# Kernel optimization log

Hardware: AMD Instinct MI355X
Metric: run time of the kernel (lower is better)

The kernel has to match this reference:

```python
import jax, jax.numpy as jnp
import numpy as np

B, N_NUC, N_UP, N_DOWN = 512, 16, 32, 32
N_ELEC = N_UP + N_DOWN            # 64 electrons
F = 8                             # edge feature dim (Gaussian RBF envelopes)
D = N_NUC * F                     # embedding_dim = 128 (positional electron embeddings)
L = 3                             # n_interactions
N_ATOM_TYPES = 4


def _rbf(diff):
    # diff: [..., 3] -> [..., F]; Gaussian RBF features of the interparticle distance
    d = jnp.sqrt(jnp.sum(diff * diff, axis=-1) + 1e-12)
    mu = jnp.linspace(0.0, 4.0, F, dtype=diff.dtype)
    return jnp.exp(-(d[..., None] - mu) ** 2)


def setup_inputs() -> dict:
    key = jax.random.key(0)
    ks = jax.random.split(key, 9)
    r = 2.0 * jax.random.normal(ks[0], (B, N_ELEC, 3), dtype=jnp.float32)
    R = 2.0 * jax.random.normal(ks[1], (B, N_NUC, 3), dtype=jnp.float32)
    atom_types = jax.random.randint(ks[2], (N_NUC,), 0, N_ATOM_TYPES)
    embed_table = 0.1 * jax.random.normal(ks[3], (N_ATOM_TYPES, D), dtype=jnp.float32)
    we_same = 0.1 * jax.random.normal(ks[4], (L, F, D), dtype=jnp.float32)
    we_anti = 0.1 * jax.random.normal(ks[5], (L, F, D), dtype=jnp.float32)
    we_ne = 0.1 * jax.random.normal(ks[6], (L, F, D), dtype=jnp.float32)
    w_up = 0.05 * jax.random.normal(ks[7], (L, 4 * D, D), dtype=jnp.float32)
    b_up = jnp.zeros((L, D), dtype=jnp.float32)
    return {
        'r': r, 'R': R, 'embed_table': embed_table,
        'we_same': we_same, 'we_anti': we_anti, 'we_ne': we_ne,
        'w_up': w_up, 'b_up': b_up, 'atom_types': atom_types,
    }


def reference(r, R, embed_table, we_same, we_anti, we_ne, w_up, b_up, atom_types):
    # --- molecular graph edge construction (pairwise differences + edge features) ---
    ee_feat = _rbf(r[:, :, None, :] - r[:, None, :, :])   # [B, e, e, F]
    ne_feat = _rbf(r[:, :, None, :] - R[:, None, :, :])   # [B, e, n, F]

    spin = jnp.arange(N_ELEC) >= N_UP
    eye = jnp.eye(N_ELEC, dtype=bool)
    same_m = ((spin[:, None] == spin[None, :]) & ~eye).astype(ee_feat.dtype)  # no self-interaction
    anti_m = (spin[:, None] != spin[None, :]).astype(ee_feat.dtype)
    feat_same = ee_feat * same_m[None, :, :, None]
    feat_anti = ee_feat * anti_m[None, :, :, None]

    # --- node factory: positional electron embeddings (dense scatter of ne features == reshape) ---
    x = ne_feat.reshape(ne_feat.shape[0], N_ELEC, N_NUC * F)  # [B, e, D]
    y = embed_table[atom_types]                               # [n, D] nuclei embeddings

    # --- message-passing layers ---
    for l in range(L):
        # messages = Linear(edge_feats) * sender embedding, summed over senders per receiver;
        # contract sender axis first to keep intermediates at [B, e, F, D]
        t_s = jnp.einsum('bijf,bjd->bifd', feat_same, x)
        z_s = jnp.einsum('bifd,fd->bid', t_s, we_same[l])
        t_a = jnp.einsum('bijf,bjd->bifd', feat_anti, x)
        z_a = jnp.einsum('bifd,fd->bid', t_a, we_anti[l])
        t_n = jnp.einsum('binf,nd->bifd', ne_feat, y)
        z_n = jnp.einsum('bifd,fd->bid', t_n, we_ne[l])
        upd = jnp.concatenate([x, z_s, z_a, z_n], axis=-1)    # [B, e, 4D]
        x = x + jnp.tanh(upd @ w_up[l] + b_up[l])
    return x  # final electron embeddings [B, N_ELEC, D]
```

## Files before the change

kernel.cpp:

```cpp
#include <hip/hip_runtime.h>


typedef unsigned short u16;
typedef __attribute__((ext_vector_type(8))) short short8;
typedef __attribute__((ext_vector_type(4))) float f32x4;

__device__ __forceinline__ u16 f2h(float f){
  return __builtin_bit_cast(u16, (_Float16)f);
}
__device__ __forceinline__ float h2f(u16 a){
  return (float)__builtin_bit_cast(_Float16, a);
}

__device__ __forceinline__ short8 rbf8(float dd){
  short8 a;
#pragma unroll
  for (int f = 0; f < 8; f++){
    float u = dd - (4.0f/7.0f)*(float)f;
    a[f] = (short)f2h(__expf(-u*u));
  }
  return a;
}

__global__ void gnn_prep(const float* __restrict__ w_up, const float* __restrict__ we_ne,
                         const float* __restrict__ embed, const int* __restrict__ atypes,
                         u16* __restrict__ wupT, u16* __restrict__ ywT){
  int id = blockIdx.x * 256 + threadIdx.x;
  if (id < 3*512*128){
    int kk = id & 511, d = (id >> 9) & 127, l = id >> 16;
    wupT[(l*128 + d)*512 + kk] = f2h(w_up[(l*512 + kk)*128 + d]);
  } else {
    id -= 3*512*128;
    int k = id & 127, d = (id >> 7) & 127, l = id >> 14;
    int n = k >> 3, f = k & 7;
    float y  = embed[atypes[n]*128 + d];
    float wn = we_ne[(l*8 + f)*128 + d];
    ywT[(l*128 + d)*128 + k] = f2h(y * wn);
  }
}

__global__ __launch_bounds__(256, 2) void gnn_main(
    const float* __restrict__ r_g, const float* __restrict__ R_g,
    const float* __restrict__ weS_g, const float* __restrict__ weA_g,
    const float* __restrict__ bup_g,
    const u16* __restrict__ wupT, const u16* __restrict__ ywT,
    float* __restrict__ out)
{
  __shared__ __attribute__((aligned(16))) u16 xb[64][136];
  __shared__ _Float16 dee[64][64];
  __shared__ _Float16 dne[64][16];
  __shared__ float bup[128];
  __shared__ __attribute__((aligned(16))) u16 arena[13824];

  const int tid  = threadIdx.x;
  const int b    = blockIdx.x;
  const int lane = tid & 63;
  const int w    = tid >> 6;
  const int col  = lane & 15;
  const int q    = lane >> 4;
  const int i0   = w * 16;
  const int s    = w >> 1;
  const int mrow = i0 + col;

  u16* const zst  = arena;
  u16* const wbuf = arena + 8704;
  u16* const buf0 = arena;
  u16* const buf1 = arena + 5120;
  u16* const mybuf = (s == 0) ? buf0 : buf1;
  const int bd = tid & 127;
  const int bg = tid >> 7;
  u16* const bbuf = (bg == 0) ? buf0 : buf1;

  {
    float* rs = (float*)arena;
    float* Rs = rs + 64*4;
    if (tid < 64){
#pragma unroll
      for (int k = 0; k < 3; k++) rs[tid*4+k] = r_g[(b*64+tid)*3 + k];
    } else if (tid < 80){
      int n = tid - 64;
#pragma unroll
      for (int k = 0; k < 3; k++) Rs[n*4+k] = R_g[(b*16+n)*3 + k];
    }
    __syncthreads();
    {
      int i = tid >> 2;
      float x0 = rs[i*4], x1 = rs[i*4+1], x2 = rs[i*4+2];
      int jb = (tid & 3) * 16;
#pragma unroll
      for (int jj = 0; jj < 16; jj++){
        int j = jb + jj;
        float dx = x0 - rs[j*4], dy = x1 - rs[j*4+1], dz = x2 - rs[j*4+2];
        dee[i][j] = (_Float16)sqrtf(dx*dx + dy*dy + dz*dz + 1e-12f);
      }
      int nb = (tid & 3) * 4;
#pragma unroll
      for (int nn = 0; nn < 4; nn++){
        int n = nb + nn;
        float dx = x0 - Rs[n*4], dy = x1 - Rs[n*4+1], dz = x2 - Rs[n*4+2];
        dne[i][n] = (_Float16)sqrtf(dx*dx + dy*dy + dz*dz + 1e-12f);
      }
    }
    __syncthreads();
    {
      int i = tid >> 2;
      int nb = (tid & 3) * 4;
#pragma unroll
      for (int nn = 0; nn < 4; nn++){
        int n = nb + nn;
        short8 p = rbf8((float)dne[i][n]);
        *(short8*)&xb[i][n*8] = p;
      }
    }
    __syncthreads();
  }

  f32x4 xr[8];
#pragma unroll
  for (int nt = 0; nt < 8; nt++)
#pragma unroll
    for (int rr = 0; rr < 4; rr++)
      xr[nt][rr] = h2f(xb[i0 + q*4 + rr][nt*16 + col]);

  const f32x4 vzero = {0.f, 0.f, 0.f, 0.f};

  for (int l = 0; l < 3; l++){
    const u16* wT_l  = wupT + (l*128)*512;
    const u16* ywT_l = ywT  + (l*128)*128;

    if (tid < 128) bup[tid] = bup_g[l*128 + tid];
    float wefS[8], wefA[8];
#pragma unroll
    for (int f = 0; f < 8; f++){
      wefS[f] = weS_g[(l*8+f)*128 + bd];
      wefA[f] = weA_g[(l*8+f)*128 + bd];
    }
    __syncthreads();

    f32x4 upd[8], zacc[8];
#pragma unroll
    for (int nt = 0; nt < 8; nt++) upd[nt] = vzero;

    for (int c = 0; c < 4; c++){
      { int d = tid >> 1, h = (tid & 1) << 4;
        const u16* src = wT_l + d*512 + 32*c + h;
        *(short8*)&wbuf[d*40 + h]     = *(const short8*)src;
        *(short8*)&wbuf[d*40 + h + 8] = *(const short8*)(src + 8); }
      __syncthreads();
      short8 a = *(const short8*)&xb[mrow][32*c + (q<<3)];
#pragma unroll
      for (int nt = 0; nt < 8; nt++){
        short8 bb = *(const short8*)&wbuf[(nt*16+col)*40 + (q<<3)];
        upd[nt] = __builtin_amdgcn_mfma_f32_16x16x32_f16(a, bb, upd[nt], 0, 0, 0);
      }
      __syncthreads();
    }

#pragma unroll 1
    for (int pass = 0; pass < 2; pass++){
      const bool same = (pass == 0);
#pragma unroll
      for (int nt = 0; nt < 8; nt++) zacc[nt] = vzero;
      for (int c = 0; c < 8; c++){
        {
          int jb = (same ? 32*bg : 32*(1-bg)) + 4*c;
#pragma unroll
          for (int jj = 0; jj < 4; jj++){
            float xv = h2f(xb[jb+jj][bd]);
            short8 p;
#pragma unroll
            for (int f = 0; f < 8; f++)
              p[f] = (short)f2h(xv * (same ? wefS[f] : wefA[f]));
            *(short8*)&bbuf[bd*40 + (jj<<3)] = p;
          }
        }
        __syncthreads();
        int j = (same ? 32*s : 32*(1-s)) + 4*c + q;
        short8 a = rbf8((float)dee[mrow][j]);
        if (same && j == mrow) a = (short8)0;
#pragma unroll
        for (int nt = 0; nt < 8; nt++){
          short8 bb = *(const short8*)&mybuf[(nt*16+col)*40 + (q<<3)];
          zacc[nt] = __builtin_amdgcn_mfma_f32_16x16x32_f16(a, bb, zacc[nt], 0, 0, 0);
        }
        __syncthreads();
      }
#pragma unroll
      for (int nt = 0; nt < 8; nt++)
#pragma unroll
        for (int rr = 0; rr < 4; rr++)
          zst[(i0 + q*4 + rr)*136 + nt*16 + col] = f2h(zacc[nt][rr]);
      __syncthreads();
      int kb0 = same ? 128 : 256;
      for (int c = 0; c < 4; c++){
        { int d = tid >> 1, h = (tid & 1) << 4;
          const u16* src = wT_l + d*512 + kb0 + 32*c + h;
          *(short8*)&wbuf[d*40 + h]     = *(const short8*)src;
          *(short8*)&wbuf[d*40 + h + 8] = *(const short8*)(src + 8); }
        __syncthreads();
        short8 a = *(const short8*)&zst[mrow*136 + 32*c + (q<<3)];
#pragma unroll
        for (int nt = 0; nt < 8; nt++){
          short8 bb = *(const short8*)&wbuf[(nt*16+col)*40 + (q<<3)];
          upd[nt] = __builtin_amdgcn_mfma_f32_16x16x32_f16(a, bb, upd[nt], 0, 0, 0);
        }
        __syncthreads();
      }
    }

#pragma unroll
    for (int nt = 0; nt < 8; nt++) zacc[nt] = vzero;
    for (int c = 0; c < 4; c++){
      { int d = tid >> 1, h = (tid & 1) << 4;
        const u16* src = ywT_l + d*128 + 32*c + h;
        *(short8*)&wbuf[d*40 + h]     = *(const short8*)src;
        *(short8*)&wbuf[d*40 + h + 8] = *(const short8*)(src + 8); }
      __syncthreads();
      int n = c*4 + q;
      short8 a = rbf8((float)dne[mrow][n]);
#pragma unroll
      for (int nt = 0; nt < 8; nt++){
        short8 bb = *(const short8*)&wbuf[(nt*16+col)*40 + (q<<3)];
        zacc[nt] = __builtin_amdgcn_mfma_f32_16x16x32_f16(a, bb, zacc[nt], 0, 0, 0);
      }
      __syncthreads();
    }
#pragma unroll
    for (int nt = 0; nt < 8; nt++)
#pragma unroll
      for (int rr = 0; rr < 4; rr++)
        zst[(i0 + q*4 + rr)*136 + nt*16 + col] = f2h(zacc[nt][rr]);
    __syncthreads();
    for (int c = 0; c < 4; c++){
      { int d = tid >> 1, h = (tid & 1) << 4;
        const u16* src = wT_l + d*512 + 384 + 32*c + h;
        *(short8*)&wbuf[d*40 + h]     = *(const short8*)src;
        *(short8*)&wbuf[d*40 + h + 8] = *(const short8*)(src + 8); }
      __syncthreads();
      short8 a = *(const short8*)&zst[mrow*136 + 32*c + (q<<3)];
#pragma unroll
      for (int nt = 0; nt < 8; nt++){
        short8 bb = *(const short8*)&wbuf[(nt*16+col)*40 + (q<<3)];
        upd[nt] = __builtin_amdgcn_mfma_f32_16x16x32_f16(a, bb, upd[nt], 0, 0, 0);
      }
      __syncthreads();
    }

#pragma unroll
    for (int nt = 0; nt < 8; nt++){
      float bb = bup[nt*16 + col];
#pragma unroll
      for (int rr = 0; rr < 4; rr++){
        float v = upd[nt][rr] + bb;
        float e = __expf(2.0f * v);
        float th = 1.0f - 2.0f * __builtin_amdgcn_rcpf(e + 1.0f);
        xr[nt][rr] += th;
      }
    }
    if (l < 2){
#pragma unroll
      for (int nt = 0; nt < 8; nt++)
#pragma unroll
        for (int rr = 0; rr < 4; rr++)
          xb[i0 + q*4 + rr][nt*16 + col] = f2h(xr[nt][rr]);
      __syncthreads();
    } else {
#pragma unroll
      for (int nt = 0; nt < 8; nt++)
#pragma unroll
        for (int rr = 0; rr < 4; rr++)
          out[(b*64 + i0 + q*4 + rr)*128 + nt*16 + col] = xr[nt][rr];
    }
  }
}

extern "C" void kernel_launch(void* const* d_in, const int* in_sizes, int n_in,
                              void* d_out, int out_size, void* d_ws, size_t ws_size,
                              hipStream_t stream){
  const float* r     = (const float*)d_in[0];
  const float* R     = (const float*)d_in[1];
  const float* embed = (const float*)d_in[2];
  const float* weS   = (const float*)d_in[3];
  const float* weA   = (const float*)d_in[4];
  const float* weN   = (const float*)d_in[5];
  const float* wup   = (const float*)d_in[6];
  const float* bup   = (const float*)d_in[7];
  const int* atyp    = (const int*)d_in[8];

  u16* wupT = (u16*)d_ws;
  u16* ywT  = wupT + 3*128*512;

  gnn_prep<<<960, 256, 0, stream>>>(wup, weN, embed, atyp, wupT, ywT);
  gnn_main<<<512, 256, 0, stream>>>(r, R, weS, weA, bup, wupT, ywT, (float*)d_out);
}
```

Measured before the change: 162.8 us.

## Stream MFMA weight operands from global and drop LDS staging barriers

The kernel no longer stages weight tiles into shared memory. Each wave now reads its MFMA B operands straight from global memory, which removes nearly all __syncthreads in the layer loop. Pairwise and nuclear distances are kept in per-lane registers instead of shared arrays. The edge-message B operand is built in registers with packed half-precision multiplies of x by the edge weights, rather than in a shared buffer. This cuts shared-memory use and barrier stalls, but each wave re-reads the weights through the cache hierarchy and register pressure goes up.

```diff
diff --git a/kernel.cpp b/kernel.cpp
--- a/kernel.cpp
+++ b/kernel.cpp
@@ -2,15 +2,14 @@
 
 
 typedef unsigned short u16;
+typedef unsigned int u32;
 typedef __attribute__((ext_vector_type(8))) short short8;
 typedef __attribute__((ext_vector_type(4))) float f32x4;
-
-__device__ __forceinline__ u16 f2h(float f){
-  return __builtin_bit_cast(u16, (_Float16)f);
-}
-__device__ __forceinline__ float h2f(u16 a){
-  return (float)__builtin_bit_cast(_Float16, a);
-}
+typedef __attribute__((ext_vector_type(4))) u32 u32x4;
+typedef _Float16 h2 __attribute__((ext_vector_type(2)));
+
+__device__ __forceinline__ u16 f2h(float f){ return __builtin_bit_cast(u16, (_Float16)f); }
+__device__ __forceinline__ float h2f(u16 a){ return (float)__builtin_bit_cast(_Float16, a); }
 
 __device__ __forceinline__ short8 rbf8(float dd){
   short8 a;
@@ -47,10 +46,7 @@
     float* __restrict__ out)
 {
   __shared__ __attribute__((aligned(16))) u16 xb[64][136];
-  __shared__ _Float16 dee[64][64];
-  __shared__ _Float16 dne[64][16];
-  __shared__ float bup[128];
-  __shared__ __attribute__((aligned(16))) u16 arena[13824];
+  __shared__ __attribute__((aligned(16))) u16 zst[64][136];
 
   const int tid  = threadIdx.x;
   const int b    = blockIdx.x;
@@ -62,18 +58,10 @@
   const int s    = w >> 1;
   const int mrow = i0 + col;
 
-  u16* const zst  = arena;
-  u16* const wbuf = arena + 8704;
-  u16* const buf0 = arena;
-  u16* const buf1 = arena + 5120;
-  u16* const mybuf = (s == 0) ? buf0 : buf1;
-  const int bd = tid & 127;
-  const int bg = tid >> 7;
-  u16* const bbuf = (bg == 0) ? buf0 : buf1;
-
+  float dS[8], dA[8], dN[4];
   {
-    float* rs = (float*)arena;
-    float* Rs = rs + 64*4;
+    float* rs = (float*)&zst[0][0];
+    float* Rs = rs + 256;
     if (tid < 64){
 #pragma unroll
       for (int k = 0; k < 3; k++) rs[tid*4+k] = r_g[(b*64+tid)*3 + k];
@@ -84,32 +72,32 @@
     }
     __syncthreads();
     {
-      int i = tid >> 2;
-      float x0 = rs[i*4], x1 = rs[i*4+1], x2 = rs[i*4+2];
-      int jb = (tid & 3) * 16;
-#pragma unroll
-      for (int jj = 0; jj < 16; jj++){
-        int j = jb + jj;
-        float dx = x0 - rs[j*4], dy = x1 - rs[j*4+1], dz = x2 - rs[j*4+2];
-        dee[i][j] = (_Float16)sqrtf(dx*dx + dy*dy + dz*dz + 1e-12f);
-      }
-      int nb = (tid & 3) * 4;
+      float x0 = rs[mrow*4], x1 = rs[mrow*4+1], x2 = rs[mrow*4+2];
+#pragma unroll
+      for (int c = 0; c < 8; c++){
+        int j = 32*s + 4*c + q;
+        float dx = x0-rs[j*4], dy = x1-rs[j*4+1], dz = x2-rs[j*4+2];
+        dS[c] = sqrtf(dx*dx + dy*dy + dz*dz + 1e-12f);
+        j = 32*(1-s) + 4*c + q;
+        dx = x0-rs[j*4]; dy = x1-rs[j*4+1]; dz = x2-rs[j*4+2];
+        dA[c] = sqrtf(dx*dx + dy*dy + dz*dz + 1e-12f);
+      }
+#pragma unroll
+      for (int c = 0; c < 4; c++){
+        int n = 4*c + q;
+        float dx = x0-Rs[n*4], dy = x1-Rs[n*4+1], dz = x2-Rs[n*4+2];
+        dN[c] = sqrtf(dx*dx + dy*dy + dz*dz + 1e-12f);
+      }
+    }
+    {
+      int i = tid >> 2, nb = (tid & 3)*4;
+      float y0 = rs[i*4], y1 = rs[i*4+1], y2 = rs[i*4+2];
 #pragma unroll
       for (int nn = 0; nn < 4; nn++){
         int n = nb + nn;
-        float dx = x0 - Rs[n*4], dy = x1 - Rs[n*4+1], dz = x2 - Rs[n*4+2];
-        dne[i][n] = (_Float16)sqrtf(dx*dx + dy*dy + dz*dz + 1e-12f);
-      }
-    }
-    __syncthreads();
-    {
-      int i = tid >> 2;
-      int nb = (tid & 3) * 4;
-#pragma unroll
-      for (int nn = 0; nn < 4; nn++){
-        int n = nb + nn;
-        short8 p = rbf8((float)dne[i][n]);
-        *(short8*)&xb[i][n*8] = p;
+        float dx = y0-Rs[n*4], dy = y1-Rs[n*4+1], dz = y2-Rs[n*4+2];
+        float dd = sqrtf(dx*dx + dy*dy + dz*dz + 1e-12f);
+        *(short8*)&xb[i][n*8] = rbf8(dd);
       }
     }
     __syncthreads();
@@ -124,140 +112,122 @@
 
   const f32x4 vzero = {0.f, 0.f, 0.f, 0.f};
 
+#pragma unroll 1
   for (int l = 0; l < 3; l++){
     const u16* wT_l  = wupT + (l*128)*512;
     const u16* ywT_l = ywT  + (l*128)*128;
 
-    if (tid < 128) bup[tid] = bup_g[l*128 + tid];
-    float wefS[8], wefA[8];
-#pragma unroll
-    for (int f = 0; f < 8; f++){
-      wefS[f] = weS_g[(l*8+f)*128 + bd];
-      wefA[f] = weA_g[(l*8+f)*128 + bd];
-    }
-    __syncthreads();
-
-    f32x4 upd[8], zacc[8];
+    float bupr[8];
+#pragma unroll
+    for (int nt = 0; nt < 8; nt++) bupr[nt] = bup_g[l*128 + nt*16 + col];
+
+    f32x4 upd[8];
 #pragma unroll
     for (int nt = 0; nt < 8; nt++) upd[nt] = vzero;
 
+#pragma unroll
     for (int c = 0; c < 4; c++){
-      { int d = tid >> 1, h = (tid & 1) << 4;
-        const u16* src = wT_l + d*512 + 32*c + h;
-        *(short8*)&wbuf[d*40 + h]     = *(const short8*)src;
-        *(short8*)&wbuf[d*40 + h + 8] = *(const short8*)(src + 8); }
-      __syncthreads();
       short8 a = *(const short8*)&xb[mrow][32*c + (q<<3)];
 #pragma unroll
       for (int nt = 0; nt < 8; nt++){
-        short8 bb = *(const short8*)&wbuf[(nt*16+col)*40 + (q<<3)];
+        short8 bb = *(const short8*)(wT_l + (nt*16+col)*512 + 32*c + (q<<3));
         upd[nt] = __builtin_amdgcn_mfma_f32_16x16x32_f16(a, bb, upd[nt], 0, 0, 0);
       }
-      __syncthreads();
     }
 
 #pragma unroll 1
     for (int pass = 0; pass < 2; pass++){
-      const bool same = (pass == 0);
+      const float* weX = pass ? weA_g : weS_g;
+      const int jb0 = pass ? 32*(1-s) : 32*s;
+      h2 wp[8][4];
+#pragma unroll
+      for (int nt = 0; nt < 8; nt++)
+#pragma unroll
+        for (int p = 0; p < 4; p++){
+          h2 t;
+          t[0] = (_Float16)weX[(l*8 + 2*p  )*128 + nt*16 + col];
+          t[1] = (_Float16)weX[(l*8 + 2*p+1)*128 + nt*16 + col];
+          wp[nt][p] = t;
+        }
+      f32x4 zacc[8];
 #pragma unroll
       for (int nt = 0; nt < 8; nt++) zacc[nt] = vzero;
+#pragma unroll
       for (int c = 0; c < 8; c++){
-        {
-          int jb = (same ? 32*bg : 32*(1-bg)) + 4*c;
-#pragma unroll
-          for (int jj = 0; jj < 4; jj++){
-            float xv = h2f(xb[jb+jj][bd]);
-            short8 p;
-#pragma unroll
-            for (int f = 0; f < 8; f++)
-              p[f] = (short)f2h(xv * (same ? wefS[f] : wefA[f]));
-            *(short8*)&bbuf[bd*40 + (jj<<3)] = p;
-          }
-        }
-        __syncthreads();
-        int j = (same ? 32*s : 32*(1-s)) + 4*c + q;
-        short8 a = rbf8((float)dee[mrow][j]);
-        if (same && j == mrow) a = (short8)0;
-#pragma unroll
-        for (int nt = 0; nt < 8; nt++){
-          short8 bb = *(const short8*)&mybuf[(nt*16+col)*40 + (q<<3)];
+        int j = jb0 + 4*c + q;
+        float dd = pass ? dA[c] : dS[c];
+        short8 a = rbf8(dd);
+        if (!pass && j == mrow) a = (short8)0;
+#pragma unroll
+        for (int nt = 0; nt < 8; nt++){
+          _Float16 xh = __builtin_bit_cast(_Float16, xb[j][nt*16 + col]);
+          h2 xd; xd[0] = xh; xd[1] = xh;
+          u32x4 bu;
+#pragma unroll
+          for (int p = 0; p < 4; p++)
+            bu[p] = __builtin_bit_cast(u32, (h2)(xd * wp[nt][p]));
+          short8 bb = __builtin_bit_cast(short8, bu);
           zacc[nt] = __builtin_amdgcn_mfma_f32_16x16x32_f16(a, bb, zacc[nt], 0, 0, 0);
         }
-        __syncthreads();
-      }
-#pragma unroll
-      for (int nt = 0; nt < 8; nt++)
-#pragma unroll
-        for (int rr = 0; rr < 4; rr++)
-          zst[(i0 + q*4 + rr)*136 + nt*16 + col] = f2h(zacc[nt][rr]);
-      __syncthreads();
-      int kb0 = same ? 128 : 256;
-      for (int c = 0; c < 4; c++){
-        { int d = tid >> 1, h = (tid & 1) << 4;
-          const u16* src = wT_l + d*512 + kb0 + 32*c + h;
-          *(short8*)&wbuf[d*40 + h]     = *(const short8*)src;
-          *(short8*)&wbuf[d*40 + h + 8] = *(const short8*)(src + 8); }
-        __syncthreads();
-        short8 a = *(const short8*)&zst[mrow*136 + 32*c + (q<<3)];
-#pragma unroll
-        for (int nt = 0; nt < 8; nt++){
-          short8 bb = *(const short8*)&wbuf[(nt*16+col)*40 + (q<<3)];
+      }
+#pragma unroll
+      for (int nt = 0; nt < 8; nt++)
+#pragma unroll
+        for (int rr = 0; rr < 4; rr++)
+          zst[i0 + q*4 + rr][nt*16 + col] = f2h(zacc[nt][rr]);
+      const int kb0 = pass ? 256 : 128;
+#pragma unroll
+      for (int c = 0; c < 4; c++){
+        short8 a = *(const short8*)&zst[mrow][32*c + (q<<3)];
+#pragma unroll
+        for (int nt = 0; nt < 8; nt++){
+          short8 bb = *(const short8*)(wT_l + (nt*16+col)*512 + kb0 + 32*c + (q<<3));
           upd[nt] = __builtin_amdgcn_mfma_f32_16x16x32_f16(a, bb, upd[nt], 0, 0, 0);
         }
-        __syncthreads();
-      }
-    }
-
-#pragma unroll
-    for (int nt = 0; nt < 8; nt++) zacc[nt] = vzero;
-    for (int c = 0; c < 4; c++){
-      { int d = tid >> 1, h = (tid & 1) << 4;
-        const u16* src = ywT_l + d*128 + 32*c + h;
-        *(short8*)&wbuf[d*40 + h]     = *(const short8*)src;
-        *(short8*)&wbuf[d*40 + h + 8] = *(const short8*)(src + 8); }
-      __syncthreads();
-      int n = c*4 + q;
-      short8 a = rbf8((float)dne[mrow][n]);
-#pragma unroll
-      for (int nt = 0; nt < 8; nt++){
-        short8 bb = *(const short8*)&wbuf[(nt*16+col)*40 + (q<<3)];
-        zacc[nt] = __builtin_amdgcn_mfma_f32_16x16x32_f16(a, bb, zacc[nt], 0, 0, 0);
-      }
-      __syncthreads();
-    }
-#pragma unroll
-    for (int nt = 0; nt < 8; nt++)
-#pragma unroll
-      for (int rr = 0; rr < 4; rr++)
-        zst[(i0 + q*4 + rr)*136 + nt*16 + col] = f2h(zacc[nt][rr]);
-    __syncthreads();
-    for (int c = 0; c < 4; c++){
-      { int d = tid >> 1, h = (tid & 1) << 4;
-        const u16* src = wT_l + d*512 + 384 + 32*c + h;
-        *(short8*)&wbuf[d*40 + h]     = *(const short8*)src;
-        *(short8*)&wbuf[d*40 + h + 8] = *(const short8*)(src + 8); }
-      __syncthreads();
-      short8 a = *(const short8*)&zst[mrow*136 + 32*c + (q<<3)];
-#pragma unroll
-      for (int nt = 0; nt < 8; nt++){
-        short8 bb = *(const short8*)&wbuf[(nt*16+col)*40 + (q<<3)];
-        upd[nt] = __builtin_amdgcn_mfma_f32_16x16x32_f16(a, bb, upd[nt], 0, 0, 0);
-      }
-      __syncthreads();
+      }
+    }
+
+    {
+      f32x4 zacc[8];
+#pragma unroll
+      for (int nt = 0; nt < 8; nt++) zacc[nt] = vzero;
+#pragma unroll
+      for (int c = 0; c < 4; c++){
+        short8 a = rbf8(dN[c]);
+#pragma unroll
+        for (int nt = 0; nt < 8; nt++){
+          short8 bb = *(const short8*)(ywT_l + (nt*16+col)*128 + 32*c + (q<<3));
+          zacc[nt] = __builtin_amdgcn_mfma_f32_16x16x32_f16(a, bb, zacc[nt], 0, 0, 0);
+        }
+      }
+#pragma unroll
+      for (int nt = 0; nt < 8; nt++)
+#pragma unroll
+        for (int rr = 0; rr < 4; rr++)
+          zst[i0 + q*4 + rr][nt*16 + col] = f2h(zacc[nt][rr]);
+#pragma unroll
+      for (int c = 0; c < 4; c++){
+        short8 a = *(const short8*)&zst[mrow][32*c + (q<<3)];
+#pragma unroll
+        for (int nt = 0; nt < 8; nt++){
+          short8 bb = *(const short8*)(wT_l + (nt*16+col)*512 + 384 + 32*c + (q<<3));
+          upd[nt] = __builtin_amdgcn_mfma_f32_16x16x32_f16(a, bb, upd[nt], 0, 0, 0);
+        }
+      }
     }
 
 #pragma unroll
     for (int nt = 0; nt < 8; nt++){
-      float bb = bup[nt*16 + col];
 #pragma unroll
       for (int rr = 0; rr < 4; rr++){
-        float v = upd[nt][rr] + bb;
+        float v = upd[nt][rr] + bupr[nt];
         float e = __expf(2.0f * v);
         float th = 1.0f - 2.0f * __builtin_amdgcn_rcpf(e + 1.0f);
         xr[nt][rr] += th;
       }
     }
     if (l < 2){
+      __syncthreads();
 #pragma unroll
       for (int nt = 0; nt < 8; nt++)
 #pragma unroll
```

Result: slower. 236.0 us (+44.9%).
